# Optimization experiments

Hardware: AMD Instinct MI355X
Metric: run time of the kernel (lower is better)

## Reference

```python
import jax, jax.numpy as jnp
import numpy as np

SMALL = -1000.0


def setup_inputs() -> dict:
    key = jax.random.key(0)
    k1, k2, k3, k4 = jax.random.split(key, 4)
    B, T, L = 1024, 512, 62          # batch, max_seq_len, emission label count
    K = L + 2                         # total labels incl. start (L) and end (L+1)
    pred = jax.random.normal(k1, (B, T, L), dtype=jnp.float32)
    ref = jax.random.randint(k2, (B, T), 0, L)
    seq_len = jnp.clip(jax.random.randint(k3, (B,), 0, T + 1), 1, T)
    transitions = jax.random.normal(k4, (K, K), dtype=jnp.float32)
    transitions = transitions.at[K - 2, :].set(-10000.0)
    transitions = transitions.at[K - 1, :].set(-10000.0)
    return {"pred": pred, "ref": ref, "seq_len": seq_len, "transitions": transitions}


def _crf_loss(pred, ref, seq_len, transitions):
    B, T, L = pred.shape
    K = L + 2
    start_id, end_id = L, L + 1
    dt = pred.dtype

    # observations: (B, T+2, K) = [b_s row, padded emissions, right padding row]
    obs = jnp.concatenate([pred, jnp.full((B, T, 2), SMALL, dtype=dt)], axis=2)
    b_s = jnp.concatenate([jnp.full((L,), SMALL, dt), jnp.array([0.0, SMALL], dt)])
    r_pad = jnp.concatenate([jnp.zeros((L,), dt), jnp.full((2,), SMALL, dt)])
    observations = jnp.concatenate(
        [jnp.broadcast_to(b_s, (B, 1, K)), obs, jnp.broadcast_to(r_pad, (B, 1, K))],
        axis=1)
    # end-of-sequence bonus added at position seq_len+1 for each example
    e_s = jnp.concatenate([jnp.full((L,), SMALL, dt), jnp.array([0.0, 1000.0], dt)])
    observations = observations.at[jnp.arange(B), seq_len + 1].add(e_s)

    # sequential forward (alpha) recurrence: logsumexp over previous label
    def step(prev, obs_t):
        # prev: (B, K), obs_t: (B, K); scores: (B, K_prev, K_next)
        scores = prev[:, :, None] + obs_t[:, None, :] + transitions
        new = jax.nn.logsumexp(scores, axis=1)
        return new, new

    init = observations[:, 0]                              # (B, K)
    xs = jnp.swapaxes(observations[:, 1:, :], 0, 1)        # (T+1, B, K)
    _, paths_scores = jax.lax.scan(step, init, xs)         # (T+1, B, K)

    final = paths_scores[seq_len, jnp.arange(B)]           # (B, K) alpha at step seq_len
    all_paths_scores = jax.nn.logsumexp(final, axis=1).sum()

    # gold path emission score
    emit_mask = (jnp.arange(T)[None, :] < seq_len[:, None]).astype(dt)   # (B, T)
    gold_emit = jnp.take_along_axis(pred, ref[:, :, None], axis=2)[..., 0]
    real_score = jnp.sum(gold_emit * emit_mask)

    # gold path transition score: [start, tags..., end]
    padded = jnp.concatenate(
        [jnp.full((B, 1), start_id, ref.dtype), ref, jnp.zeros((B, 1), ref.dtype)],
        axis=1)                                            # (B, T+2)
    padded = padded.at[jnp.arange(B), seq_len + 1].set(end_id)
    trans_mask = (jnp.arange(T + 1)[None, :] < (seq_len + 1)[:, None]).astype(dt)
    gold_trans = transitions[padded[:, :-1], padded[:, 1:]]  # (B, T+1)
    real_score = real_score + jnp.sum(gold_trans * trans_mask)

    return all_paths_scores - real_score


def reference(pred, ref, seq_len, transitions):
    return _crf_loss(pred, ref, seq_len, transitions)
```

## Files before the change

kernel.cpp:

```cpp
#include <hip/hip_runtime.h>


#define SMALLF   (-1000.0f)
#define LOG2E_F  1.4426950408889634f
#define LN2_F    0.6931471805599453f

#if defined(__has_builtin)
#if __has_builtin(__builtin_amdgcn_exp2f)
#define EXP2F(x) __builtin_amdgcn_exp2f(x)
#else
#define EXP2F(x) exp2f(x)
#endif
#if __has_builtin(__builtin_amdgcn_logf)
#define LOG2F(x) __builtin_amdgcn_logf(x)
#else
#define LOG2F(x) log2f(x)
#endif
#else
#define EXP2F(x) exp2f(x)
#define LOG2F(x) log2f(x)
#endif

typedef _Float16 h2 __attribute__((ext_vector_type(2)));

#if defined(__has_builtin) && __has_builtin(__builtin_amdgcn_fdot2)
#define FDOT2(a, b, c) __builtin_amdgcn_fdot2((a), (b), (c), false)
#else
#define FDOT2(a, b, c) fmaf((float)(a).x, (float)(b).x, \
                            fmaf((float)(a).y, (float)(b).y, (c)))
#endif

#define MEMFENCE() asm volatile("" ::: "memory")

__device__ __forceinline__ float bcast_first(float v) {
    return __uint_as_float(__builtin_amdgcn_readfirstlane(__float_as_uint(v)));
}

__device__ __forceinline__ float step_scale(float ss, int& Ci) {
    const float s0 = bcast_first(ss);
    const int ex = (int)((__float_as_uint(s0) >> 23) & 0xFF) - 127;
    Ci += ex + 6;
    return __uint_as_float((unsigned)(127 - ex - 6) << 23);
}

__device__ __forceinline__ float dot62(const _Float16* __restrict__ hsh,
                                       const h2* __restrict__ Eh) {
    const float4* q4 = (const float4*)hsh;
    float4 v[8];
#pragma unroll
    for (int r = 0; r < 8; ++r) v[r] = q4[r];
    float a0 = 0.f, a1 = 0.f, a2 = 0.f, a3 = 0.f;
#pragma unroll
    for (int r = 0; r < 8; ++r) {
        const h2 p0 = __builtin_bit_cast(h2, v[r].x);
        const h2 p1 = __builtin_bit_cast(h2, v[r].y);
        const h2 p2 = __builtin_bit_cast(h2, v[r].z);
        const h2 p3 = __builtin_bit_cast(h2, v[r].w);
        a0 = FDOT2(p0, Eh[4 * r + 0], a0);
        a1 = FDOT2(p1, Eh[4 * r + 1], a1);
        a2 = FDOT2(p2, Eh[4 * r + 2], a2);
        if (4 * r + 3 < 31)
            a3 = FDOT2(p3, Eh[4 * r + 3], a3);
    }
    return (a0 + a1) + (a2 + a3);
}

__global__ __launch_bounds__(64, 1) void crf_fused_kernel(
    const float* __restrict__ pred,
    const int*   __restrict__ ref,
    const int*   __restrict__ seq_len,
    const float* __restrict__ trans,
    float*       __restrict__ out,
    int T, int L)
{
    const int b    = blockIdx.x;
    const int lane = threadIdx.x;
    const int slen = seq_len[b];
    const int nmid = slen - 1;
    const float* prow = pred + (size_t)b * T * L;
    const int*   rrow = ref  + (size_t)b * T;
    const bool mine = (lane < 62);

    __shared__ __align__(16) _Float16 hsh[64];

    int cidx[8], pidx[8];
#pragma unroll
    for (int k = 0; k < 8; ++k) {
        const int t = lane + (k << 6);
        cidx[k] = (t < slen) ? rrow[t] : 0;
        pidx[k] = (t >= 1 && t < slen) ? rrow[t - 1] : 0;
    }
    float gacc = 0.f;
#pragma unroll
    for (int k = 0; k < 8; ++k) {
        const int t = lane + (k << 6);
        if (t < slen) {
            gacc += prow[(size_t)t * L + cidx[k]];
            if (t >= 1) gacc += trans[(pidx[k] << 6) + cidx[k]];
        }
    }
    if (lane == 0)
        gacc += trans[(62 << 6) + rrow[0]] + trans[(rrow[slen - 1] << 6) + 63];

    h2 Eh[31];
    float psum = 0.f;
#pragma unroll
    for (int k = 0; k < 31; ++k) {
        const float e0 = EXP2F(trans[(2 * k + 0) * 64 + lane] * LOG2E_F);
        const float e1 = EXP2F(trans[(2 * k + 1) * 64 + lane] * LOG2E_F);
        Eh[k].x = (_Float16)e0; Eh[k].y = (_Float16)e1;
        psum += e0 + e1;
    }

    float cur[8];
#pragma unroll
    for (int u = 0; u < 8; ++u) {
        const int row = (u + 1 < T) ? (u + 1) : (T - 1);
        cur[u] = mine ? prow[(size_t)row * L + lane] : 0.f;
    }

    int Ci = 0;
    const float c_base = SMALLF * LOG2E_F;
    _Float16 hval;
    {
        const float q0 = psum * EXP2F((mine ? prow[lane] : 0.f) * LOG2E_F);
        const float sc = step_scale(q0, Ci);
        hval = (_Float16)(q0 * sc);
    }

    const int nfull = nmid >> 3;
    const int rem   = nmid & 7;
    for (int c = 0; c < nfull; ++c) {
        float W[8], nxt[8];
#pragma unroll
        for (int u = 0; u < 8; ++u)
            W[u] = EXP2F(cur[u] * LOG2E_F);
        const int base = 8 * (c + 1) + 1;
#pragma unroll
        for (int u = 0; u < 8; ++u) {
            const int row = (base + u < T) ? (base + u) : (T - 1);
            nxt[u] = mine ? prow[(size_t)row * L + lane] : 0.f;
        }
#pragma unroll
        for (int u = 0; u < 8; ++u) {
            MEMFENCE();
            hsh[lane] = hval;
            MEMFENCE();
            const float ss = dot62(hsh, Eh);
            const float sc = step_scale(ss, Ci);
            hval = (_Float16)(ss * (W[u] * sc));
        }
#pragma unroll
        for (int u = 0; u < 8; ++u) cur[u] = nxt[u];
    }

    float Wr[7];
#pragma unroll
    for (int u = 0; u < 7; ++u)
        Wr[u] = EXP2F(cur[u] * LOG2E_F);
#pragma unroll
    for (int u = 0; u < 7; ++u) {
        if (u < rem) {
            MEMFENCE();
            hsh[lane] = hval;
            MEMFENCE();
            const float ss = dot62(hsh, Eh);
            const float sc = step_scale(ss, Ci);
            hval = (_Float16)(ss * (Wr[u] * sc));
        }
    }

    {
        MEMFENCE();
        hsh[lane] = hval;
        MEMFENCE();
        const float ssf = dot62(hsh, Eh);
        const float pvf = (slen < T) ? cur[rem] : 0.f;
        float ob;
        if (lane < 62)       ob = pvf + SMALLF;
        else if (lane == 62) ob = SMALLF;
        else                 ob = 0.f;
        const float alpha = c_base + (float)Ci + LOG2F(ssf) + ob * LOG2E_F;

        float mx = alpha;
#pragma unroll
        for (int k = 32; k >= 1; k >>= 1)
            mx = fmaxf(mx, __shfl_xor(mx, k, 64));
        float pe = EXP2F(alpha - mx);
#pragma unroll
        for (int k = 32; k >= 1; k >>= 1)
            pe += __shfl_xor(pe, k, 64);
#pragma unroll
        for (int k = 32; k >= 1; k >>= 1)
            gacc += __shfl_xor(gacc, k, 64);

        if (lane == 0) {
            const float logZ2 = mx + LOG2F(pe);
            atomicAdd(out, LN2_F * logZ2 - gacc);
        }
    }
}

extern "C" void kernel_launch(void* const* d_in, const int* in_sizes, int n_in,
                              void* d_out, int out_size, void* d_ws, size_t ws_size,
                              hipStream_t stream) {
    const float* pred  = (const float*)d_in[0];
    const int*   ref   = (const int*)  d_in[1];
    const int*   slen  = (const int*)  d_in[2];
    const float* trans = (const float*)d_in[3];

    const int B = in_sizes[2];
    const int T = in_sizes[1] / B;
    const int L = in_sizes[0] / in_sizes[1];

    hipMemsetAsync(d_out, 0, sizeof(float), stream);
    crf_fused_kernel<<<B, 64, 0, stream>>>(pred, ref, slen, trans,
                                           (float*)d_out, T, L);
}
```

Measured before the change: 261.7 us.

## Replace LDS broadcast in CRF recurrence with DPP and permlane cross-lane exchange

Each forward step no longer writes the scaled alpha vector to shared memory and reads all 64 values back. Instead the values are packed to fp16 pairs, spread within groups of 16 lanes using DPP moves, and each lane computes four partial dot products that are combined with permlane16/32 swaps. The transition exponentials are re-laid out into four register arrays to match this distribution, and the initial psum is rebuilt the same way. The goal is to remove the LDS round trip latency from the serial critical path, at the cost of more VALU and cross-lane instructions per step, plus a reliance on permlane swap semantics being detected correctly at runtime.

New measurement: 265.4 us. No clear change (+1.4%).

```diff
diff --git a/kernel.cpp b/kernel.cpp
--- a/kernel.cpp
+++ b/kernel.cpp
@@ -30,7 +30,32 @@
                             fmaf((float)(a).y, (float)(b).y, (c)))
 #endif
 
-#define MEMFENCE() asm volatile("" ::: "memory")
+template <int CTRL>
+__device__ __forceinline__ unsigned dppmov(unsigned v) {
+    return (unsigned)__builtin_amdgcn_update_dpp((int)v, (int)v, CTRL, 0xF, 0xF, false);
+}
+#define DPP_QP_X1 0xB1
+#define DPP_QP_X2 0x4E
+#define DPP_ROR4  0x124
+#define DPP_ROR8  0x128
+#define DPP_ROR12 0x12C
+
+__device__ __forceinline__ unsigned x4sel(unsigned v, bool b2) {
+    const unsigned a = dppmov<DPP_ROR4>(v);
+    const unsigned b = dppmov<DPP_ROR12>(v);
+    return b2 ? a : b;
+}
+
+__device__ __forceinline__ unsigned x16(unsigned v, bool sel) {
+    unsigned a = v, b = v;
+    asm("v_permlane16_swap_b32 %0, %1" : "+v"(a), "+v"(b));
+    return sel ? a : b;
+}
+__device__ __forceinline__ unsigned x32(unsigned v, bool sel) {
+    unsigned a = v, b = v;
+    asm("v_permlane32_swap_b32 %0, %1" : "+v"(a), "+v"(b));
+    return sel ? a : b;
+}
 
 __device__ __forceinline__ float bcast_first(float v) {
     return __uint_as_float(__builtin_amdgcn_readfirstlane(__float_as_uint(v)));
@@ -43,26 +68,35 @@
     return __uint_as_float((unsigned)(127 - ex - 6) << 23);
 }
 
-__device__ __forceinline__ float dot62(const _Float16* __restrict__ hsh,
-                                       const h2* __restrict__ Eh) {
-    const float4* q4 = (const float4*)hsh;
-    float4 v[8];
-#pragma unroll
-    for (int r = 0; r < 8; ++r) v[r] = q4[r];
-    float a0 = 0.f, a1 = 0.f, a2 = 0.f, a3 = 0.f;
-#pragma unroll
-    for (int r = 0; r < 8; ++r) {
-        const h2 p0 = __builtin_bit_cast(h2, v[r].x);
-        const h2 p1 = __builtin_bit_cast(h2, v[r].y);
-        const h2 p2 = __builtin_bit_cast(h2, v[r].z);
-        const h2 p3 = __builtin_bit_cast(h2, v[r].w);
-        a0 = FDOT2(p0, Eh[4 * r + 0], a0);
-        a1 = FDOT2(p1, Eh[4 * r + 1], a1);
-        a2 = FDOT2(p2, Eh[4 * r + 2], a2);
-        if (4 * r + 3 < 31)
-            a3 = FDOT2(p3, Eh[4 * r + 3], a3);
-    }
-    return (a0 + a1) + (a2 + a3);
+__device__ __forceinline__ float step_ss(float hf,
+                                         const h2* __restrict__ EhA,
+                                         const h2* __restrict__ EhB,
+                                         const h2* __restrict__ EhC,
+                                         const h2* __restrict__ EhD,
+                                         bool b2, bool s16, bool s32) {
+    const unsigned n1 = dppmov<DPP_QP_X1>(__float_as_uint(hf));
+    unsigned r[8];
+    r[0] = __builtin_bit_cast(unsigned,
+              __builtin_amdgcn_cvt_pkrtz(hf, __uint_as_float(n1)));
+    r[1] = dppmov<DPP_QP_X2>(r[0]);
+    r[2] = x4sel(r[0], b2);
+    r[3] = x4sel(r[1], b2);
+    r[4] = dppmov<DPP_ROR8>(r[0]);
+    r[5] = dppmov<DPP_ROR8>(r[1]);
+    r[6] = dppmov<DPP_ROR8>(r[2]);
+    r[7] = dppmov<DPP_ROR8>(r[3]);
+    float pA = 0.f, pB = 0.f, pC = 0.f, pD = 0.f;
+#pragma unroll
+    for (int k = 0; k < 8; ++k) {
+        const h2 v = __builtin_bit_cast(h2, r[k]);
+        pA = FDOT2(v, EhA[k], pA);
+        pB = FDOT2(v, EhB[k], pB);
+        pC = FDOT2(v, EhC[k], pC);
+        pD = FDOT2(v, EhD[k], pD);
+    }
+    const float A  = pA + __uint_as_float(x16(__float_as_uint(pB), s16));
+    const float A2 = pC + __uint_as_float(x16(__float_as_uint(pD), s16));
+    return A + __uint_as_float(x32(__float_as_uint(A2), s32));
 }
 
 __global__ __launch_bounds__(64, 1) void crf_fused_kernel(
@@ -74,26 +108,24 @@
     int T, int L)
 {
     const int b    = blockIdx.x;
-    const int lane = threadIdx.x;
+    const unsigned lane = threadIdx.x;
     const int slen = seq_len[b];
     const int nmid = slen - 1;
     const float* prow = pred + (size_t)b * T * L;
     const int*   rrow = ref  + (size_t)b * T;
     const bool mine = (lane < 62);
 
-    __shared__ __align__(16) _Float16 hsh[64];
-
     int cidx[8], pidx[8];
 #pragma unroll
     for (int k = 0; k < 8; ++k) {
-        const int t = lane + (k << 6);
+        const int t = (int)lane + (k << 6);
         cidx[k] = (t < slen) ? rrow[t] : 0;
         pidx[k] = (t >= 1 && t < slen) ? rrow[t - 1] : 0;
     }
     float gacc = 0.f;
 #pragma unroll
     for (int k = 0; k < 8; ++k) {
-        const int t = lane + (k << 6);
+        const int t = (int)lane + (k << 6);
         if (t < slen) {
             gacc += prow[(size_t)t * L + cidx[k]];
             if (t >= 1) gacc += trans[(pidx[k] << 6) + cidx[k]];
@@ -102,15 +134,52 @@
     if (lane == 0)
         gacc += trans[(62 << 6) + rrow[0]] + trans[(rrow[slen - 1] << 6) + 63];
 
-    h2 Eh[31];
-    float psum = 0.f;
-#pragma unroll
-    for (int k = 0; k < 31; ++k) {
-        const float e0 = EXP2F(trans[(2 * k + 0) * 64 + lane] * LOG2E_F);
-        const float e1 = EXP2F(trans[(2 * k + 1) * 64 + lane] * LOG2E_F);
-        Eh[k].x = (_Float16)e0; Eh[k].y = (_Float16)e1;
-        psum += e0 + e1;
-    }
+    const bool b2 = (lane & 4u) != 0;
+    bool flip16 = false, flip32 = false;
+    {
+        const unsigned p = x16(lane, ((lane >> 4) & 1u) != 0);
+        if (__builtin_amdgcn_readfirstlane((int)p) == 0) flip16 = true;
+        const unsigned q = x32(lane, ((lane >> 5) & 1u) != 0);
+        if (__builtin_amdgcn_readfirstlane((int)q) == 0) flip32 = true;
+    }
+    const bool s16 = ((((lane >> 4) & 1u) != 0) != flip16);
+    const bool s32 = ((((lane >> 5) & 1u) != 0) != flip32);
+    const unsigned m16 = x16(lane, s16);
+    const unsigned m32 = x32(lane, s32);
+    const unsigned cD  = x16(m32, s16);
+
+    unsigned gp[8];
+    gp[0] = lane | (dppmov<DPP_QP_X1>(lane) << 16);
+    gp[1] = dppmov<DPP_QP_X2>(gp[0]);
+    gp[2] = x4sel(gp[0], b2);
+    gp[3] = x4sel(gp[1], b2);
+    gp[4] = dppmov<DPP_ROR8>(gp[0]);
+    gp[5] = dppmov<DPP_ROR8>(gp[1]);
+    gp[6] = dppmov<DPP_ROR8>(gp[2]);
+    gp[7] = dppmov<DPP_ROR8>(gp[3]);
+
+    h2 EhA[8], EhB[8], EhC[8], EhD[8];
+    float sA = 0.f, sB = 0.f, sC = 0.f, sD = 0.f;
+#pragma unroll
+    for (int k = 0; k < 8; ++k) {
+        const unsigned rlo = gp[k] & 0xFFFFu;
+        const unsigned rhi = gp[k] >> 16;
+        const float a0 = EXP2F(trans[rlo * 64u + lane] * LOG2E_F);
+        const float a1 = EXP2F(trans[rhi * 64u + lane] * LOG2E_F);
+        EhA[k].x = (_Float16)a0; EhA[k].y = (_Float16)a1; sA += a0 + a1;
+        const float b0 = EXP2F(trans[rlo * 64u + m16] * LOG2E_F);
+        const float b1 = EXP2F(trans[rhi * 64u + m16] * LOG2E_F);
+        EhB[k].x = (_Float16)b0; EhB[k].y = (_Float16)b1; sB += b0 + b1;
+        const float c0 = EXP2F(trans[rlo * 64u + m32] * LOG2E_F);
+        const float c1 = EXP2F(trans[rhi * 64u + m32] * LOG2E_F);
+        EhC[k].x = (_Float16)c0; EhC[k].y = (_Float16)c1; sC += c0 + c1;
+        const float d0 = EXP2F(trans[rlo * 64u + cD] * LOG2E_F);
+        const float d1 = EXP2F(trans[rhi * 64u + cD] * LOG2E_F);
+        EhD[k].x = (_Float16)d0; EhD[k].y = (_Float16)d1; sD += d0 + d1;
+    }
+    const float psA  = sA + __uint_as_float(x16(__float_as_uint(sB), s16));
+    const float psA2 = sC + __uint_as_float(x16(__float_as_uint(sD), s16));
+    const float psum = psA + __uint_as_float(x32(__float_as_uint(psA2), s32));
 
     float cur[8];
 #pragma unroll
@@ -121,11 +190,11 @@
 
     int Ci = 0;
     const float c_base = SMALLF * LOG2E_F;
-    _Float16 hval;
+    float hf;
     {
         const float q0 = psum * EXP2F((mine ? prow[lane] : 0.f) * LOG2E_F);
         const float sc = step_scale(q0, Ci);
-        hval = (_Float16)(q0 * sc);
+        hf = q0 * sc;
     }
 
     const int nfull = nmid >> 3;
@@ -143,12 +212,9 @@
         }
 #pragma unroll
         for (int u = 0; u < 8; ++u) {
-            MEMFENCE();
-            hsh[lane] = hval;
-            MEMFENCE();
-            const float ss = dot62(hsh, Eh);
+            const float ss = step_ss(hf, EhA, EhB, EhC, EhD, b2, s16, s32);
             const float sc = step_scale(ss, Ci);
-            hval = (_Float16)(ss * (W[u] * sc));
+            hf = ss * (W[u] * sc);
         }
 #pragma unroll
         for (int u = 0; u < 8; ++u) cur[u] = nxt[u];
@@ -161,20 +227,14 @@
 #pragma unroll
     for (int u = 0; u < 7; ++u) {
         if (u < rem) {
-            MEMFENCE();
-            hsh[lane] = hval;
-            MEMFENCE();
-            const float ss = dot62(hsh, Eh);
+            const float ss = step_ss(hf, EhA, EhB, EhC, EhD, b2, s16, s32);
             const float sc = step_scale(ss, Ci);
-            hval = (_Float16)(ss * (Wr[u] * sc));
+            hf = ss * (Wr[u] * sc);
         }
     }
 
     {
-        MEMFENCE();
-        hsh[lane] = hval;
-        MEMFENCE();
-        const float ssf = dot62(hsh, Eh);
+        const float ssf = step_ss(hf, EhA, EhB, EhC, EhD, b2, s16, s32);
         const float pvf = (slen < T) ? cur[rem] : 0.f;
         float ob;
         if (lane < 62)       ob = pvf + SMALLF;
```
